# Kernel tuning notes

Measured on AMD Instinct MI355X. Metric: run time of the kernel, lower is better.

Reference implementation:

```python
import jax, jax.numpy as jnp
import numpy as np

N_NODES = 100000


def _gcn_layer(x, W, b, src, dst, n):
    # symmetric normalization (add_self_loops=False): deg = in-degree at dst
    deg = jax.ops.segment_sum(jnp.ones_like(src, dtype=x.dtype), dst, num_segments=n)
    dis = jnp.where(deg > 0, jax.lax.rsqrt(jnp.maximum(deg, 1.0)), 0.0)
    h = x @ W                                    # [N, out]
    norm = dis[src] * dis[dst]                   # [E]
    msg = h[src] * norm[:, None]                 # [E, out]
    out = jax.ops.segment_sum(msg, dst, num_segments=n)
    return out + b


def setup_inputs() -> dict:
    key = jax.random.key(0)
    k1, k2, k3, k4, k5, k6 = jax.random.split(key, 6)
    F_IN, HID, OUT = 64, 64, 2
    x = jax.random.normal(k1, (N_NODES, F_IN), dtype=jnp.float32)
    edge_index = jax.random.randint(k2, (2, 1600000), 0, N_NODES, dtype=jnp.int64)
    s1 = 1.0 / np.sqrt(2 * F_IN)
    s2 = 1.0 / np.sqrt(HID)
    W1 = jax.random.uniform(k3, (2 * F_IN, HID), jnp.float32, -s1, s1)
    b1 = jax.random.uniform(k4, (HID,), jnp.float32, -s1, s1)
    W2 = jax.random.uniform(k5, (HID, OUT), jnp.float32, -s2, s2)
    b2 = jax.random.uniform(k6, (OUT,), jnp.float32, -s2, s2)
    return {"x": x, "edge_index": edge_index, "W1": W1, "b1": b1, "W2": W2, "b2": b2}


def reference(x, edge_index, W1, b1, W2, b2):
    n = x.shape[0]
    src, dst = edge_index[0], edge_index[1]
    # global mean pool broadcast to every node, concat on feature dim -> [N, 2F]
    mean = jnp.mean(x, axis=0, keepdims=True)
    complete = jnp.concatenate([x, jnp.broadcast_to(mean, x.shape)], axis=1)
    h = _gcn_layer(complete, W1, b1, src, dst, n)
    h = jax.nn.relu(h)
    out = _gcn_layer(h, W2, b2, src, dst, n)
    return out
```

## Files before the change

kernel.cpp:

```cpp
#include <hip/hip_runtime.h>


#define NPB        256
#define NPB_SHIFT  8
#define BKTS       512
#define BKT_CAP    5120
#define CHUNK      4096
#define EPT        8
#define CS_BLK     64
#define CUR_STRIDE 32

using bf16x8 = __attribute__((ext_vector_type(8))) short;
using f32x4  = __attribute__((ext_vector_type(4))) float;

__device__ __forceinline__ unsigned short f2bf(float v) {
    unsigned u = __float_as_uint(v);
    u += 0x7FFFu + ((u >> 16) & 1u);
    return (unsigned short)(u >> 16);
}
__device__ __forceinline__ float bf2f(unsigned short h) {
    return __uint_as_float((unsigned)h << 16);
}
__device__ __forceinline__ float bfu_lo(unsigned u) { return __uint_as_float(u << 16); }
__device__ __forceinline__ float bfu_hi(unsigned u) { return __uint_as_float(u & 0xFFFF0000u); }

__global__ __launch_bounds__(512) void bucketAC_kernel(
        const int* __restrict__ src, const int* __restrict__ dst,
        int e, unsigned* __restrict__ pairs, int* __restrict__ cursor,
        const float* __restrict__ x, float* __restrict__ sums,
        const float* __restrict__ W1, unsigned short* __restrict__ wtg, int n) {
    int tid = threadIdx.x;
    if (blockIdx.x < CS_BLK) {
        __shared__ float4 s4[512];
        int cb = blockIdx.x;
        const float4* x4 = (const float4*)x;
        int total4 = n * 16;
        float4 acc = make_float4(0.f, 0.f, 0.f, 0.f);
        for (int i = cb * 512 + tid; i < total4; i += CS_BLK * 512) {
            float4 v = x4[i];
            acc.x += v.x; acc.y += v.y; acc.z += v.z; acc.w += v.w;
        }
        s4[tid] = acc;
        __syncthreads();
        if (tid < 16) {
            float4 v = s4[tid];
            for (int k = 1; k < 32; ++k) {
                float4 w = s4[tid + 16 * k];
                v.x += w.x; v.y += w.y; v.z += w.z; v.w += w.w;
            }
            atomicAdd(&sums[tid * 4 + 0], v.x);
            atomicAdd(&sums[tid * 4 + 1], v.y);
            atomicAdd(&sums[tid * 4 + 2], v.z);
            atomicAdd(&sums[tid * 4 + 3], v.w);
        }
        return;
    }
    if (blockIdx.x == CS_BLK) {
        for (int i = tid; i < 4096; i += 512) {
            int k = i >> 6, j = i & 63;
            wtg[j * 64 + k] = f2bf(W1[k * 64 + j]);
        }
        return;
    }
    __shared__ int cnt[BKTS], sb[BKTS], gpos[BKTS];
    __shared__ unsigned stage[CHUNK];
    __shared__ unsigned short bb[CHUNK];
    int chunkStart = (blockIdx.x - CS_BLK - 1) * CHUNK;
    int v = e - chunkStart;
    if (v > CHUNK) v = CHUNK;
    cnt[tid] = 0;
    __syncthreads();
    int myb[EPT], myoff[EPT];
    unsigned myp[EPT];
#pragma unroll
    for (int t = 0; t < EPT; ++t) {
        int i = chunkStart + t * 512 + tid;
        myb[t] = -1;
        if (i < e) {
            int s = src[i], d = dst[i];
            myb[t] = d >> NPB_SHIFT;
            myp[t] = ((unsigned)s << NPB_SHIFT) | (unsigned)(d & (NPB - 1));
            myoff[t] = atomicAdd(&cnt[myb[t]], 1);
        }
    }
    __syncthreads();
    sb[tid] = cnt[tid];
    __syncthreads();
    for (int off = 1; off < BKTS; off <<= 1) {
        int t = (tid >= off) ? sb[tid - off] : 0;
        __syncthreads();
        sb[tid] += t;
        __syncthreads();
    }
    {
        int excl = tid ? sb[tid - 1] : 0;
        int cb = cnt[tid];
        if (cb > 0) {
            int gb = atomicAdd(&cursor[tid * CUR_STRIDE], cb);
            gpos[tid] = tid * BKT_CAP + gb - excl;
        }
        cnt[tid] = excl;
    }
    __syncthreads();
#pragma unroll
    for (int t = 0; t < EPT; ++t) {
        if (myb[t] >= 0) {
            int p = cnt[myb[t]] + myoff[t];
            stage[p] = myp[t];
            bb[p] = (unsigned short)myb[t];
        }
    }
    __syncthreads();
    for (int j = tid; j < v; j += 512) {
        int bk = bb[j];
        int wi = gpos[bk] + j;
        if (wi < (bk + 1) * BKT_CAP) pairs[wi] = stage[j];
    }
}

__global__ __launch_bounds__(512) void csrB_kernel(
        const unsigned* __restrict__ pairs, const int* __restrict__ cursor,
        float* __restrict__ dis, int* __restrict__ rowstart,
        int* __restrict__ eidx, int n,
        const float* __restrict__ sums, const float* __restrict__ W1,
        float* __restrict__ cvec) {
    __shared__ int ldeg[NPB];
    __shared__ int lcur[NPB];
    __shared__ int scanbuf[512];
    __shared__ int s_ebase;
    int b = blockIdx.x;
    int tid = threadIdx.x;
    int node0 = b << NPB_SHIFT;
    if (node0 >= n) return;
    int nl = n - node0;
    if (nl > NPB) nl = NPB;
    int cnt_b = cursor[b * CUR_STRIDE];
    if (cnt_b > BKT_CAP) cnt_b = BKT_CAP;
    if (tid < NPB) ldeg[tid] = 0;
    if (tid == 0) s_ebase = 0;
    __syncthreads();
    if (tid < b) atomicAdd(&s_ebase, cursor[tid * CUR_STRIDE]);
    const unsigned* mp = pairs + (size_t)b * BKT_CAP;
    for (int i = tid; i < cnt_b; i += 512)
        atomicAdd(&ldeg[mp[i] & (NPB - 1)], 1);
    __syncthreads();
    scanbuf[tid] = (tid < NPB) ? ldeg[tid] : 0;
    __syncthreads();
    for (int off = 1; off < 512; off <<= 1) {
        int t = (tid >= off) ? scanbuf[tid - off] : 0;
        __syncthreads();
        scanbuf[tid] += t;
        __syncthreads();
    }
    int ebase = s_ebase;
    if (tid < NPB) {
        int ex = tid ? scanbuf[tid - 1] : 0;
        lcur[tid] = ex;
        if (tid < nl) {
            int dv = ldeg[tid];
            rowstart[node0 + tid] = ebase + ex;
            dis[node0 + tid] = dv > 0 ? rsqrtf((float)dv) : 0.f;
        }
    }
    if (tid == 0 && node0 + NPB >= n)
        rowstart[n] = ebase + cnt_b;
    __syncthreads();
    for (int i = tid; i < cnt_b; i += 512) {
        unsigned p = mp[i];
        int pos = atomicAdd(&lcur[p & (NPB - 1)], 1);
        eidx[ebase + pos] = (int)(p >> NPB_SHIFT);
    }
    if (b == 0 && tid < 64) {
        float inv_n = 1.0f / (float)n;
        float acc = 0.f;
        for (int k = 0; k < 64; ++k) acc += (sums[k] * inv_n) * W1[(64 + k) * 64 + tid];
        cvec[tid] = acc;
    }
}

__global__ __launch_bounds__(256) void gemm1_kernel(
        const float* __restrict__ x, const unsigned short* __restrict__ wtg,
        const float* __restrict__ c, const float* __restrict__ dis,
        unsigned short* __restrict__ h1s, int n) {
    __shared__ unsigned short Xs[64 * 72];
    __shared__ unsigned short Ws[64 * 72];
    int tid = threadIdx.x;
    int row0 = blockIdx.x * 64;
    for (int i = tid; i < 1024; i += 256) {
        int j = i >> 4, k4 = (i & 15) * 4;
        *(ushort4*)&Ws[j * 72 + k4] = *(const ushort4*)&wtg[j * 64 + k4];
    }
    for (int i = tid; i < 1024; i += 256) {
        int r = i >> 4, k4 = (i & 15) * 4;
        int gr = row0 + r;
        float4 xv = make_float4(0.f, 0.f, 0.f, 0.f);
        if (gr < n) xv = *(const float4*)&x[(size_t)gr * 64 + k4];
        ushort4 hv;
        hv.x = f2bf(xv.x); hv.y = f2bf(xv.y); hv.z = f2bf(xv.z); hv.w = f2bf(xv.w);
        *(ushort4*)&Xs[r * 72 + k4] = hv;
    }
    __syncthreads();
    int lane = tid & 63;
    int wv = tid >> 6;
    int l15 = lane & 15;
    int quad = lane >> 4;
    f32x4 acc0 = {0.f, 0.f, 0.f, 0.f}, acc1 = acc0, acc2 = acc0, acc3 = acc0;
    int xrow = wv * 16 + l15;
#pragma unroll
    for (int ks = 0; ks < 2; ++ks) {
        bf16x8 bfrag = *(const bf16x8*)&Xs[xrow * 72 + ks * 32 + quad * 8];
        bf16x8 a0 = *(const bf16x8*)&Ws[(0 * 16 + l15) * 72 + ks * 32 + quad * 8];
        bf16x8 a1 = *(const bf16x8*)&Ws[(1 * 16 + l15) * 72 + ks * 32 + quad * 8];
        bf16x8 a2 = *(const bf16x8*)&Ws[(2 * 16 + l15) * 72 + ks * 32 + quad * 8];
        bf16x8 a3 = *(const bf16x8*)&Ws[(3 * 16 + l15) * 72 + ks * 32 + quad * 8];
        acc0 = __builtin_amdgcn_mfma_f32_16x16x32_bf16(a0, bfrag, acc0, 0, 0, 0);
        acc1 = __builtin_amdgcn_mfma_f32_16x16x32_bf16(a1, bfrag, acc1, 0, 0, 0);
        acc2 = __builtin_amdgcn_mfma_f32_16x16x32_bf16(a2, bfrag, acc2, 0, 0, 0);
        acc3 = __builtin_amdgcn_mfma_f32_16x16x32_bf16(a3, bfrag, acc3, 0, 0, 0);
    }
    int grow = row0 + xrow;
    if (grow < n) {
        float dv = dis[grow];
        const float4* c4 = (const float4*)c;
        f32x4 accs[4] = {acc0, acc1, acc2, acc3};
#pragma unroll
        for (int t = 0; t < 4; ++t) {
            float4 cj = c4[t * 4 + quad];
            ushort4 hs;
            hs.x = f2bf((accs[t][0] + cj.x) * dv);
            hs.y = f2bf((accs[t][1] + cj.y) * dv);
            hs.z = f2bf((accs[t][2] + cj.z) * dv);
            hs.w = f2bf((accs[t][3] + cj.w) * dv);
            *(ushort4*)&h1s[(size_t)grow * 64 + t * 16 + quad * 4] = hs;
        }
    }
}

__global__ void gather1_kernel(const int* __restrict__ rowstart,
                               const int* __restrict__ eidx, const float* __restrict__ dis,
                               const unsigned short* __restrict__ h1s,
                               const float* __restrict__ b1, const float* __restrict__ W2,
                               float* __restrict__ h2s, int n) {
    int lane = threadIdx.x & 63;
    int node = blockIdx.x * 4 + (threadIdx.x >> 6);
    if (node >= n) return;
    int rs = rowstart[node];
    int re = rowstart[node + 1];
    int dn = re - rs;
    int m = dn < 64 ? dn : 64;
    int eHeld = (lane < m) ? eidx[rs + lane] : 0;
    int sub = lane >> 5;
    int fp  = (lane & 31) * 2;
    float ax = 0.f, ay = 0.f;
    int j = 0;
    for (; j + 16 <= m; j += 16) {
        int s0 = __shfl(eHeld, j + 0 + sub, 64);
        int s1 = __shfl(eHeld, j + 2 + sub, 64);
        int s2 = __shfl(eHeld, j + 4 + sub, 64);
        int s3 = __shfl(eHeld, j + 6 + sub, 64);
        int s4 = __shfl(eHeld, j + 8 + sub, 64);
        int s5 = __shfl(eHeld, j + 10 + sub, 64);
        int s6 = __shfl(eHeld, j + 12 + sub, 64);
        int s7 = __shfl(eHeld, j + 14 + sub, 64);
        unsigned u0 = *(const unsigned*)&h1s[((size_t)s0 << 6) + fp];
        unsigned u1 = *(const unsigned*)&h1s[((size_t)s1 << 6) + fp];
        unsigned u2 = *(const unsigned*)&h1s[((size_t)s2 << 6) + fp];
        unsigned u3 = *(const unsigned*)&h1s[((size_t)s3 << 6) + fp];
        unsigned u4 = *(const unsigned*)&h1s[((size_t)s4 << 6) + fp];
        unsigned u5 = *(const unsigned*)&h1s[((size_t)s5 << 6) + fp];
        unsigned u6 = *(const unsigned*)&h1s[((size_t)s6 << 6) + fp];
        unsigned u7 = *(const unsigned*)&h1s[((size_t)s7 << 6) + fp];
        ax += (bfu_lo(u0) + bfu_lo(u1)) + (bfu_lo(u2) + bfu_lo(u3))
            + (bfu_lo(u4) + bfu_lo(u5)) + (bfu_lo(u6) + bfu_lo(u7));
        ay += (bfu_hi(u0) + bfu_hi(u1)) + (bfu_hi(u2) + bfu_hi(u3))
            + (bfu_hi(u4) + bfu_hi(u5)) + (bfu_hi(u6) + bfu_hi(u7));
    }
    for (; j + 8 <= m; j += 8) {
        int s0 = __shfl(eHeld, j + 0 + sub, 64);
        int s1 = __shfl(eHeld, j + 2 + sub, 64);
        int s2 = __shfl(eHeld, j + 4 + sub, 64);
        int s3 = __shfl(eHeld, j + 6 + sub, 64);
        unsigned u0 = *(const unsigned*)&h1s[((size_t)s0 << 6) + fp];
        unsigned u1 = *(const unsigned*)&h1s[((size_t)s1 << 6) + fp];
        unsigned u2 = *(const unsigned*)&h1s[((size_t)s2 << 6) + fp];
        unsigned u3 = *(const unsigned*)&h1s[((size_t)s3 << 6) + fp];
        ax += (bfu_lo(u0) + bfu_lo(u1)) + (bfu_lo(u2) + bfu_lo(u3));
        ay += (bfu_hi(u0) + bfu_hi(u1)) + (bfu_hi(u2) + bfu_hi(u3));
    }
    for (; j + 4 <= m; j += 4) {
        int s0 = __shfl(eHeld, j + 0 + sub, 64);
        int s1 = __shfl(eHeld, j + 2 + sub, 64);
        unsigned u0 = *(const unsigned*)&h1s[((size_t)s0 << 6) + fp];
        unsigned u1 = *(const unsigned*)&h1s[((size_t)s1 << 6) + fp];
        ax += bfu_lo(u0) + bfu_lo(u1);
        ay += bfu_hi(u0) + bfu_hi(u1);
    }
    for (; j < m; j += 2) {
        int jj = j + sub;
        int s = __shfl(eHeld, jj < m ? jj : 0, 64);
        if (jj < m) {
            unsigned u = *(const unsigned*)&h1s[((size_t)s << 6) + fp];
            ax += bfu_lo(u);
            ay += bfu_hi(u);
        }
    }
    for (int t = 64; t < dn; ++t) {
        if (sub == 0) {
            int s = eidx[rs + t];
            unsigned u = *(const unsigned*)&h1s[((size_t)s << 6) + fp];
            ax += bfu_lo(u);
            ay += bfu_hi(u);
        }
    }
    ax += __shfl_xor(ax, 32, 64);
    ay += __shfl_xor(ay, 32, 64);
    float di = dis[node];
    float2 bv = ((const float2*)b1)[lane & 31];
    float4 w = ((const float4*)W2)[lane & 31];
    float t0 = fmaxf(di * ax + bv.x, 0.f);
    float t1 = fmaxf(di * ay + bv.y, 0.f);
    float v0 = t0 * w.x + t1 * w.z;
    float v1 = t0 * w.y + t1 * w.w;
#pragma unroll
    for (int off = 1; off <= 16; off <<= 1) {
        v0 += __shfl_xor(v0, off, 64);
        v1 += __shfl_xor(v1, off, 64);
    }
    if (lane == 0) {
        h2s[(size_t)node * 2 + 0] = di * v0;
        h2s[(size_t)node * 2 + 1] = di * v1;
    }
}

__global__ void gather2_kernel(const int* __restrict__ rowstart,
                               const int* __restrict__ eidx, const float* __restrict__ dis,
                               const float2* __restrict__ h2s, const float* __restrict__ b2,
                               float2* __restrict__ out, int n) {
    int tid = threadIdx.x;
    int node = blockIdx.x * 16 + (tid >> 4);
    if (node >= n) return;
    int el = tid & 15;
    int rs = rowstart[node];
    int dn = rowstart[node + 1] - rs;
    float ax = 0.f, ay = 0.f;
    for (int t = el; t < dn; t += 16) {
        int s = eidx[rs + t];
        float2 h = h2s[s];
        ax += h.x;
        ay += h.y;
    }
#pragma unroll
    for (int off = 1; off <= 8; off <<= 1) {
        ax += __shfl_xor(ax, off, 64);
        ay += __shfl_xor(ay, off, 64);
    }
    if (el == 0) {
        float di = dis[node];
        out[node] = make_float2(di * ax + b2[0], di * ay + b2[1]);
    }
}

extern "C" void kernel_launch(void* const* d_in, const int* in_sizes, int n_in,
                              void* d_out, int out_size, void* d_ws, size_t ws_size,
                              hipStream_t stream) {
    const float* x  = (const float*)d_in[0];
    const int*   ei = (const int*)d_in[1];
    const float* W1 = (const float*)d_in[2];
    const float* b1 = (const float*)d_in[3];
    const float* W2 = (const float*)d_in[4];
    const float* b2 = (const float*)d_in[5];
    float2* out = (float2*)d_out;

    const int n = in_sizes[0] / 64;
    const int e = in_sizes[1] / 2;
    const int* srcI = ei;
    const int* dstI = ei + e;
    const int nbkt = (n + NPB - 1) >> NPB_SHIFT;

    char* p = (char*)d_ws;
    int* rowstart = (int*)p;    p += ((size_t)(n + 1) * 4 + 255) & ~255ull;
    float* dis    = (float*)p;  p += ((size_t)n * 4 + 255) & ~255ull;
    float* sums   = (float*)p;
    int* cursor   = (int*)(p + 256);
    size_t zsize  = 256 + (size_t)nbkt * CUR_STRIDE * 4;
    char* zbase   = p;          p += (zsize + 255) & ~255ull;
    float* cvec   = (float*)p;  p += 256;
    unsigned short* wtg = (unsigned short*)p;  p += (4096 * 2 + 255) & ~255ull;
    int* eidx     = (int*)p;    p += ((size_t)e * 4 + 255) & ~255ull;
    unsigned* pairs      = (unsigned*)p;
    unsigned short* h1s  = (unsigned short*)p;
    {
        size_t pairs_sz = (size_t)nbkt * BKT_CAP * 4;
        size_t h1s_sz   = (size_t)n * 64 * 2;
        size_t u = pairs_sz > h1s_sz ? pairs_sz : h1s_sz;
        p += (u + 255) & ~255ull;
    }
    float* h2s    = (float*)p;

    hipMemsetAsync(zbase, 0, zsize, stream);

    const int nchunks = (e + CHUNK - 1) / CHUNK;

    bucketAC_kernel<<<CS_BLK + 1 + nchunks, 512, 0, stream>>>(srcI, dstI, e, pairs, cursor,
                                                              x, sums, W1, wtg, n);
    csrB_kernel<<<nbkt, 512, 0, stream>>>(pairs, cursor, dis, rowstart, eidx, n,
                                          sums, W1, cvec);
    gemm1_kernel<<<(n + 63) / 64, 256, 0, stream>>>(x, wtg, cvec, dis, h1s, n);
    gather1_kernel<<<(n + 3) / 4, 256, 0, stream>>>(rowstart, eidx, dis, h1s, b1, W2, h2s, n);
    gather2_kernel<<<(n + 15) / 16, 256, 0, stream>>>(rowstart, eidx, dis, (const float2*)h2s,
                                                      b2, out, n);
}
```

Before: 186.7 us.

## Fuse layer-1 GEMM into CSR build kernel, per-bucket node tiles

Merges the standalone gemm1 kernel into the CSR construction kernel: each 256-node bucket block now computes its degrees, then runs the bf16 MFMA transform for its own 256 rows using the locally computed dis values and a per-block recomputed mean-projection vector. This removes one kernel launch and the global round-trip of dis/cvec. Because h1s can no longer alias the pairs buffer, which is still being read, it gets its own workspace region. In exchange, every block redundantly recomputes the 64x64 cvec product, and the CSR kernel now uses more shared memory and does more work per block, which may lower occupancy.

```diff
diff --git a/kernel.cpp b/kernel.cpp
--- a/kernel.cpp
+++ b/kernel.cpp
@@ -17,9 +17,6 @@
     unsigned u = __float_as_uint(v);
     u += 0x7FFFu + ((u >> 16) & 1u);
     return (unsigned short)(u >> 16);
-}
-__device__ __forceinline__ float bf2f(unsigned short h) {
-    return __uint_as_float((unsigned)h << 16);
 }
 __device__ __forceinline__ float bfu_lo(unsigned u) { return __uint_as_float(u << 16); }
 __device__ __forceinline__ float bfu_hi(unsigned u) { return __uint_as_float(u & 0xFFFF0000u); }
@@ -118,20 +115,24 @@
     }
 }
 
-__global__ __launch_bounds__(512) void csrB_kernel(
+__global__ __launch_bounds__(512) void csrBG_kernel(
         const unsigned* __restrict__ pairs, const int* __restrict__ cursor,
         float* __restrict__ dis, int* __restrict__ rowstart,
         int* __restrict__ eidx, int n,
         const float* __restrict__ sums, const float* __restrict__ W1,
-        float* __restrict__ cvec) {
+        const unsigned short* __restrict__ wtg, const float* __restrict__ x,
+        unsigned short* __restrict__ h1s) {
     __shared__ int ldeg[NPB];
     __shared__ int lcur[NPB];
     __shared__ int scanbuf[512];
     __shared__ int s_ebase;
+    __shared__ __align__(16) float cv[64];
+    __shared__ unsigned short Ws[64 * 72];
+    __shared__ unsigned short Xs[2][64 * 72];
+    float* disl = (float*)ldeg;
     int b = blockIdx.x;
     int tid = threadIdx.x;
     int node0 = b << NPB_SHIFT;
-    if (node0 >= n) return;
     int nl = n - node0;
     if (nl > NPB) nl = NPB;
     int cnt_b = cursor[b * CUR_STRIDE];
@@ -153,85 +154,85 @@
         __syncthreads();
     }
     int ebase = s_ebase;
+    int mydeg = 0;
     if (tid < NPB) {
         int ex = tid ? scanbuf[tid - 1] : 0;
         lcur[tid] = ex;
-        if (tid < nl) {
-            int dv = ldeg[tid];
-            rowstart[node0 + tid] = ebase + ex;
-            dis[node0 + tid] = dv > 0 ? rsqrtf((float)dv) : 0.f;
-        }
+        mydeg = ldeg[tid];
+        if (tid < nl) rowstart[node0 + tid] = ebase + ex;
     }
     if (tid == 0 && node0 + NPB >= n)
         rowstart[n] = ebase + cnt_b;
     __syncthreads();
+    if (tid < NPB) {
+        float dv = mydeg > 0 ? rsqrtf((float)mydeg) : 0.f;
+        disl[tid] = dv;
+        if (tid < nl) dis[node0 + tid] = dv;
+    }
     for (int i = tid; i < cnt_b; i += 512) {
         unsigned p = mp[i];
         int pos = atomicAdd(&lcur[p & (NPB - 1)], 1);
         eidx[ebase + pos] = (int)(p >> NPB_SHIFT);
     }
-    if (b == 0 && tid < 64) {
+    if (tid < 64) {
         float inv_n = 1.0f / (float)n;
         float acc = 0.f;
         for (int k = 0; k < 64; ++k) acc += (sums[k] * inv_n) * W1[(64 + k) * 64 + tid];
-        cvec[tid] = acc;
-    }
-}
-
-__global__ __launch_bounds__(256) void gemm1_kernel(
-        const float* __restrict__ x, const unsigned short* __restrict__ wtg,
-        const float* __restrict__ c, const float* __restrict__ dis,
-        unsigned short* __restrict__ h1s, int n) {
-    __shared__ unsigned short Xs[64 * 72];
-    __shared__ unsigned short Ws[64 * 72];
-    int tid = threadIdx.x;
-    int row0 = blockIdx.x * 64;
-    for (int i = tid; i < 1024; i += 256) {
+        cv[tid] = acc;
+    }
+    for (int i = tid; i < 1024; i += 512) {
         int j = i >> 4, k4 = (i & 15) * 4;
         *(ushort4*)&Ws[j * 72 + k4] = *(const ushort4*)&wtg[j * 64 + k4];
     }
-    for (int i = tid; i < 1024; i += 256) {
-        int r = i >> 4, k4 = (i & 15) * 4;
-        int gr = row0 + r;
-        float4 xv = make_float4(0.f, 0.f, 0.f, 0.f);
-        if (gr < n) xv = *(const float4*)&x[(size_t)gr * 64 + k4];
-        ushort4 hv;
-        hv.x = f2bf(xv.x); hv.y = f2bf(xv.y); hv.z = f2bf(xv.z); hv.w = f2bf(xv.w);
-        *(ushort4*)&Xs[r * 72 + k4] = hv;
-    }
-    __syncthreads();
     int lane = tid & 63;
     int wv = tid >> 6;
+    int tile = wv >> 2;
+    int w4 = wv & 3;
     int l15 = lane & 15;
     int quad = lane >> 4;
-    f32x4 acc0 = {0.f, 0.f, 0.f, 0.f}, acc1 = acc0, acc2 = acc0, acc3 = acc0;
-    int xrow = wv * 16 + l15;
-#pragma unroll
-    for (int ks = 0; ks < 2; ++ks) {
-        bf16x8 bfrag = *(const bf16x8*)&Xs[xrow * 72 + ks * 32 + quad * 8];
-        bf16x8 a0 = *(const bf16x8*)&Ws[(0 * 16 + l15) * 72 + ks * 32 + quad * 8];
-        bf16x8 a1 = *(const bf16x8*)&Ws[(1 * 16 + l15) * 72 + ks * 32 + quad * 8];
-        bf16x8 a2 = *(const bf16x8*)&Ws[(2 * 16 + l15) * 72 + ks * 32 + quad * 8];
-        bf16x8 a3 = *(const bf16x8*)&Ws[(3 * 16 + l15) * 72 + ks * 32 + quad * 8];
-        acc0 = __builtin_amdgcn_mfma_f32_16x16x32_bf16(a0, bfrag, acc0, 0, 0, 0);
-        acc1 = __builtin_amdgcn_mfma_f32_16x16x32_bf16(a1, bfrag, acc1, 0, 0, 0);
-        acc2 = __builtin_amdgcn_mfma_f32_16x16x32_bf16(a2, bfrag, acc2, 0, 0, 0);
-        acc3 = __builtin_amdgcn_mfma_f32_16x16x32_bf16(a3, bfrag, acc3, 0, 0, 0);
-    }
-    int grow = row0 + xrow;
-    if (grow < n) {
-        float dv = dis[grow];
-        const float4* c4 = (const float4*)c;
-        f32x4 accs[4] = {acc0, acc1, acc2, acc3};
-#pragma unroll
-        for (int t = 0; t < 4; ++t) {
-            float4 cj = c4[t * 4 + quad];
-            ushort4 hs;
-            hs.x = f2bf((accs[t][0] + cj.x) * dv);
-            hs.y = f2bf((accs[t][1] + cj.y) * dv);
-            hs.z = f2bf((accs[t][2] + cj.z) * dv);
-            hs.w = f2bf((accs[t][3] + cj.w) * dv);
-            *(ushort4*)&h1s[(size_t)grow * 64 + t * 16 + quad * 4] = hs;
+#pragma unroll
+    for (int it = 0; it < 2; ++it) {
+        __syncthreads();
+        for (int i = tid; i < 2048; i += 512) {
+            int r = i >> 4, k4 = (i & 15) * 4;
+            int gr = node0 + it * 128 + r;
+            float4 xv = make_float4(0.f, 0.f, 0.f, 0.f);
+            if (gr < n) xv = *(const float4*)&x[(size_t)gr * 64 + k4];
+            ushort4 hv;
+            hv.x = f2bf(xv.x); hv.y = f2bf(xv.y); hv.z = f2bf(xv.z); hv.w = f2bf(xv.w);
+            *(ushort4*)&Xs[r >> 6][(r & 63) * 72 + k4] = hv;
+        }
+        __syncthreads();
+        int xrow = w4 * 16 + l15;
+        f32x4 acc0 = {0.f, 0.f, 0.f, 0.f}, acc1 = acc0, acc2 = acc0, acc3 = acc0;
+#pragma unroll
+        for (int ks = 0; ks < 2; ++ks) {
+            bf16x8 bfrag = *(const bf16x8*)&Xs[tile][xrow * 72 + ks * 32 + quad * 8];
+            bf16x8 a0 = *(const bf16x8*)&Ws[(0 * 16 + l15) * 72 + ks * 32 + quad * 8];
+            bf16x8 a1 = *(const bf16x8*)&Ws[(1 * 16 + l15) * 72 + ks * 32 + quad * 8];
+            bf16x8 a2 = *(const bf16x8*)&Ws[(2 * 16 + l15) * 72 + ks * 32 + quad * 8];
+            bf16x8 a3 = *(const bf16x8*)&Ws[(3 * 16 + l15) * 72 + ks * 32 + quad * 8];
+            acc0 = __builtin_amdgcn_mfma_f32_16x16x32_bf16(a0, bfrag, acc0, 0, 0, 0);
+            acc1 = __builtin_amdgcn_mfma_f32_16x16x32_bf16(a1, bfrag, acc1, 0, 0, 0);
+            acc2 = __builtin_amdgcn_mfma_f32_16x16x32_bf16(a2, bfrag, acc2, 0, 0, 0);
+            acc3 = __builtin_amdgcn_mfma_f32_16x16x32_bf16(a3, bfrag, acc3, 0, 0, 0);
+        }
+        int lrow = it * 128 + tile * 64 + xrow;
+        int grow = node0 + lrow;
+        if (grow < n) {
+            float dv = disl[lrow];
+            const float4* c4 = (const float4*)cv;
+            f32x4 accs[4] = {acc0, acc1, acc2, acc3};
+#pragma unroll
+            for (int t = 0; t < 4; ++t) {
+                float4 cj = c4[t * 4 + quad];
+                ushort4 hs;
+                hs.x = f2bf((accs[t][0] + cj.x) * dv);
+                hs.y = f2bf((accs[t][1] + cj.y) * dv);
+                hs.z = f2bf((accs[t][2] + cj.z) * dv);
+                hs.w = f2bf((accs[t][3] + cj.w) * dv);
+                *(ushort4*)&h1s[(size_t)grow * 64 + t * 16 + quad * 4] = hs;
+            }
         }
     }
 }
@@ -384,17 +385,10 @@
     int* cursor   = (int*)(p + 256);
     size_t zsize  = 256 + (size_t)nbkt * CUR_STRIDE * 4;
     char* zbase   = p;          p += (zsize + 255) & ~255ull;
-    float* cvec   = (float*)p;  p += 256;
     unsigned short* wtg = (unsigned short*)p;  p += (4096 * 2 + 255) & ~255ull;
     int* eidx     = (int*)p;    p += ((size_t)e * 4 + 255) & ~255ull;
-    unsigned* pairs      = (unsigned*)p;
-    unsigned short* h1s  = (unsigned short*)p;
-    {
-        size_t pairs_sz = (size_t)nbkt * BKT_CAP * 4;
-        size_t h1s_sz   = (size_t)n * 64 * 2;
-        size_t u = pairs_sz > h1s_sz ? pairs_sz : h1s_sz;
-        p += (u + 255) & ~255ull;
-    }
+    unsigned* pairs = (unsigned*)p;  p += ((size_t)nbkt * BKT_CAP * 4 + 255) & ~255ull;
+    unsigned short* h1s = (unsigned short*)p;  p += ((size_t)n * 64 * 2 + 255) & ~255ull;
     float* h2s    = (float*)p;
 
     hipMemsetAsync(zbase, 0, zsize, stream);
@@ -403,9 +397,8 @@
 
     bucketAC_kernel<<<CS_BLK + 1 + nchunks, 512, 0, stream>>>(srcI, dstI, e, pairs, cursor,
                                                               x, sums, W1, wtg, n);
-    csrB_kernel<<<nbkt, 512, 0, stream>>>(pairs, cursor, dis, rowstart, eidx, n,
-                                          sums, W1, cvec);
-    gemm1_kernel<<<(n + 63) / 64, 256, 0, stream>>>(x, wtg, cvec, dis, h1s, n);
+    csrBG_kernel<<<nbkt, 512, 0, stream>>>(pairs, cursor, dis, rowstart, eidx, n,
+                                           sums, W1, wtg, x, h1s);
     gather1_kernel<<<(n + 3) / 4, 256, 0, stream>>>(rowstart, eidx, dis, h1s, b1, W2, h2s, n);
     gather2_kernel<<<(n + 15) / 16, 256, 0, stream>>>(rowstart, eidx, dis, (const float2*)h2s,
                                                       b2, out, n);
```

Measured after the change: 185.7 us. Within noise of the previous version (-0.5%).
